# Kernel optimization log

Measured on AMD Instinct MI355X. Metric: run time of the kernel, lower is better.

## Reference

```python
import jax, jax.numpy as jnp
import numpy as np

B, S, H = 2, 1024, 2048
NH, NKV, HD = 16, 8, 128
N_REP = NH // NKV
EPS = 1e-6
ROPE_THETA = 1000000.0


def act_quant(x):
    # per-token int8 absmax quantization (BitNet)
    scale = 127.0 / jnp.clip(jnp.max(jnp.abs(x), axis=-1, keepdims=True), 1e-5, None)
    return jnp.clip(jnp.round(x * scale), -128.0, 127.0) / scale


def weight_quant(w):
    # ternary weight quantization via mean absmax (BitNet 1.58b)
    scale = 1.0 / jnp.clip(jnp.mean(jnp.abs(w)), 1e-5, None)
    return jnp.clip(jnp.round(w * scale), -1.0, 1.0) / scale


def bitlinear(x, w):
    # straight-through estimator: forward quantized, backward identity
    xq = x + jax.lax.stop_gradient(act_quant(x) - x)
    wq = w + jax.lax.stop_gradient(weight_quant(w) - w)
    return xq @ wq.T


def rmsnorm(x, weight):
    return weight * (x * jax.lax.rsqrt(jnp.mean(x * x, axis=-1, keepdims=True) + EPS))


def rotate_half(x):
    h = x.shape[-1] // 2
    return jnp.concatenate([-x[..., h:], x[..., :h]], axis=-1)


def setup_inputs() -> dict:
    key = jax.random.key(0)
    ks = jax.random.split(key, 6)
    x = jax.random.normal(ks[0], (B, S, H), jnp.float32)
    wq = jax.random.normal(ks[1], (NH * HD, H), jnp.float32) * 0.02
    wk = jax.random.normal(ks[2], (NKV * HD, H), jnp.float32) * 0.02
    wv = jax.random.normal(ks[3], (NKV * HD, H), jnp.float32) * 0.02
    wo = jax.random.normal(ks[4], (H, NH * HD), jnp.float32) * 0.02
    qn = jnp.ones((HD,), jnp.float32)
    kn = jnp.ones((HD,), jnp.float32)
    # real RoPE tables: [S, HD]
    inv_freq = 1.0 / (ROPE_THETA ** (jnp.arange(0, HD, 2, dtype=jnp.float32) / HD))
    freqs = jnp.outer(jnp.arange(S, dtype=jnp.float32), inv_freq)
    emb = jnp.concatenate([freqs, freqs], axis=-1)
    return dict(x=x, cos=jnp.cos(emb), sin=jnp.sin(emb),
                wq=wq, wk=wk, wv=wv, wo=wo, qn=qn, kn=kn)


def reference(x, cos, sin, wq, wk, wv, wo, qn, kn):
    b, s, _ = x.shape
    q = bitlinear(x, wq).reshape(b, s, NH, HD)
    k = bitlinear(x, wk).reshape(b, s, NKV, HD)
    v = bitlinear(x, wv).reshape(b, s, NKV, HD)
    # per-head QK RMSNorm
    q = rmsnorm(q, qn)
    k = rmsnorm(k, kn)
    # RoPE: cos/sin [S, HD] -> unsqueeze head dim -> [S, 1, HD]
    c = cos[:, None, :]
    sn = sin[:, None, :]
    q = q * c + rotate_half(q) * sn
    k = k * c + rotate_half(k) * sn
    # GQA expand: [b,s,NKV,HD] -> [b,s,NH,HD], adjacent copies per kv head
    k = jnp.repeat(k, N_REP, axis=2)
    v = jnp.repeat(v, N_REP, axis=2)
    # to [b, h, s, d]
    q = q.transpose(0, 2, 1, 3)
    k = k.transpose(0, 2, 1, 3)
    v = v.transpose(0, 2, 1, 3)
    scores = jnp.einsum('bhqd,bhkd->bhqk', q, k) / np.float32(np.sqrt(HD))
    causal = jnp.tril(jnp.ones((s, s), bool))
    scores = jnp.where(causal, scores, jnp.finfo(scores.dtype).min)
    probs = jax.nn.softmax(scores, axis=-1)
    out = jnp.einsum('bhqk,bhkd->bhqd', probs, v)
    out = out.transpose(0, 2, 1, 3).reshape(b, s, NH * HD)
    return bitlinear(out, wo)
```

## Files before the change

### kernel.cpp

```cpp
#include <hip/hip_runtime.h>
#include <hip/hip_bf16.h>

#define TT   2048
#define HH   2048
#define SEQ  1024
#define NHQ  16
#define NKVH 8
#define HDD  128

typedef __attribute__((ext_vector_type(8))) short short8;
typedef __attribute__((ext_vector_type(4))) float f32x4;
typedef __attribute__((ext_vector_type(4))) int int4v;
typedef _Float16 half8 __attribute__((ext_vector_type(8)));

static __device__ __forceinline__ unsigned short f2h(float f) {
  union { _Float16 h; unsigned short u; } c;
  c.h = (_Float16)f;
  return c.u;
}
static __device__ __forceinline__ half8 s2h(short8 v) {
  union { short8 s; half8 h; } c;
  c.s = v;
  return c.h;
}

#define GLD_LDS16(gp, lp)                                                        \
  __builtin_amdgcn_global_load_lds(                                              \
      (const __attribute__((address_space(1))) void*)(const void*)(gp),          \
      (__attribute__((address_space(3))) void*)(void*)(lp), 16, 0, 0)

__global__ __launch_bounds__(256) void k_quant_stats(const float* __restrict__ x,
                                                     signed char* __restrict__ xq,
                                                     float* __restrict__ as_inv,
                                                     const float* __restrict__ wq,
                                                     const float* __restrict__ wk,
                                                     const float* __restrict__ wv,
                                                     const float* __restrict__ wo,
                                                     double* __restrict__ part) {
  int tid = threadIdx.x;
  int wave = tid >> 6, lane = tid & 63;
  __shared__ double redd[256];
  __shared__ float wred[4];

  if (blockIdx.x < 2048) {
    int row = blockIdx.x;
    const float4* xr4 = (const float4*)(x + (size_t)row * HH);
    float4 a = xr4[tid * 2], b = xr4[tid * 2 + 1];
    float am = fmaxf(fmaxf(fmaxf(fabsf(a.x), fabsf(a.y)), fmaxf(fabsf(a.z), fabsf(a.w))),
                     fmaxf(fmaxf(fabsf(b.x), fabsf(b.y)), fmaxf(fabsf(b.z), fabsf(b.w))));
#pragma unroll
    for (int o = 32; o; o >>= 1) am = fmaxf(am, __shfl_xor(am, o));
    if (lane == 0) wred[wave] = am;
    __syncthreads();
    am = fmaxf(fmaxf(wred[0], wred[1]), fmaxf(wred[2], wred[3]));
    am = fmaxf(am, 1e-5f);
    if (tid == 0) as_inv[row] = am / 127.f;
    float scale = 127.f / am;
    float vals[8] = {a.x, a.y, a.z, a.w, b.x, b.y, b.z, b.w};
    unsigned int u0 = 0, u1 = 0;
#pragma unroll
    for (int j = 0; j < 4; ++j) {
      int q = (int)fminf(fmaxf(rintf(vals[j] * scale), -128.f), 127.f);
      u0 |= (unsigned int)(q & 255) << (8 * j);
    }
#pragma unroll
    for (int j = 0; j < 4; ++j) {
      int q = (int)fminf(fmaxf(rintf(vals[4 + j] * scale), -128.f), 127.f);
      u1 |= (unsigned int)(q & 255) << (8 * j);
    }
    uint2 uu; uu.x = u0; uu.y = u1;
    ((uint2*)(xq + (size_t)row * HH))[tid] = uu;
  } else {
    int idx = blockIdx.x - 2048;
    int wid = idx >> 8, sub = idx & 255;
    const float* w = (wid == 0) ? wq : (wid == 1) ? wk : (wid == 2) ? wv : wo;
    int nq = ((wid == 0 || wid == 3) ? 4194304 : 2097152) >> 2;
    double s = 0.0;
    for (int i = sub * 256 + tid; i < nq; i += 256 * 256) {
      float4 v = ((const float4*)w)[i];
      s += (double)fabsf(v.x) + (double)fabsf(v.y) + (double)fabsf(v.z) + (double)fabsf(v.w);
    }
    redd[tid] = s;
    __syncthreads();
    for (int st = 128; st > 0; st >>= 1) {
      if (tid < st) redd[tid] += redd[tid + st];
      __syncthreads();
    }
    if (tid == 0) part[wid * 256 + sub] = redd[0];
  }
}

__global__ __launch_bounds__(256) void k_wquant_all(const float* __restrict__ wq,
                                                    const float* __restrict__ wk,
                                                    const float* __restrict__ wv,
                                                    signed char* __restrict__ wqk,
                                                    signed char* __restrict__ wvt,
                                                    const double* __restrict__ part,
                                                    float* __restrict__ wsc) {
  int tid = threadIdx.x;
  int wave = tid >> 6, lane = tid & 63;
  __shared__ double wred[4][4];
  __shared__ float s_wsc[4];
  const double nvals[4] = {4194304.0, 2097152.0, 2097152.0, 4194304.0};
#pragma unroll
  for (int w = 0; w < 4; ++w) {
    double s = part[w * 256 + tid];
#pragma unroll
    for (int o = 32; o; o >>= 1) s += __shfl_xor(s, o);
    if (lane == 0) wred[w][wave] = s;
  }
  __syncthreads();
  if (tid < 4) {
    double s = (wred[tid][0] + wred[tid][1]) + (wred[tid][2] + wred[tid][3]);
    float v = fmaxf((float)(s / nvals[tid]), 1e-5f);
    s_wsc[tid] = v;
    if (blockIdx.x == 0) wsc[tid] = v;
  }
  __syncthreads();
  float inv0 = 1.f / s_wsc[0], inv1 = 1.f / s_wsc[1], inv2 = 1.f / s_wsc[2];

  const int NQ = 2097152;
  for (int qi = blockIdx.x * 256 + tid; qi < NQ; qi += gridDim.x * 256) {
    const float* src; signed char* dst; float inv; int off;
    if (qi < 1048576)      { src = wq; dst = wqk;           off = qi;           inv = inv0; }
    else if (qi < 1572864) { src = wk; dst = wqk + 4194304; off = qi - 1048576; inv = inv1; }
    else                   { src = wv; dst = wvt;           off = qi - 1572864; inv = inv2; }
    float4 v = ((const float4*)src)[off];
    unsigned int u = 0;
    float vv[4] = {v.x, v.y, v.z, v.w};
#pragma unroll
    for (int j = 0; j < 4; ++j) {
      int q = (int)fminf(fmaxf(rintf(vv[j] * inv), -1.f), 1.f);
      u |= (unsigned int)(q & 255) << (8 * j);
    }
    ((unsigned int*)dst)[off] = u;
  }
}

__global__ __launch_bounds__(256) void k_gemm_i8(const signed char* __restrict__ A0,
                                                 const signed char* __restrict__ B0,
                                                 const signed char* __restrict__ B1,
                                                 unsigned short* __restrict__ dh,
                                                 const float* __restrict__ asx,
                                                 const float* __restrict__ wsc,
                                                 const float* __restrict__ qn,
                                                 const float* __restrict__ kn,
                                                 const float* __restrict__ cs,
                                                 const float* __restrict__ sn,
                                                 unsigned short* __restrict__ qf,
                                                 unsigned short* __restrict__ kf) {
  const int K = HH;
  __shared__ signed char As[2][16384];
  __shared__ signed char Bs[2][16384];
  int tid = threadIdx.x;
  int wave = tid >> 6, lane = tid & 63, l15 = lane & 15, g = lane >> 4;
  int wm = wave >> 1, wn = wave & 1;

  int gid = (blockIdx.x & 7) * 64 + (blockIdx.x >> 3);
  const signed char *Ap, *Bp;
  int bm, bn, mode;
  if (gid < 384) { mode = 0; bm = (gid / 24) * 128; bn = (gid % 24) * 128; Ap = A0; Bp = B0; }
  else { mode = 1; int vid = gid - 384; bm = (vid >> 4) * 128; bn = (vid & 15) * 128; Ap = B1; Bp = A0; }

#define GSTAGE(K0, BUF)                                                               \
  {                                                                                   \
    _Pragma("unroll")                                                                 \
    for (int r = 0; r < 4; ++r) {                                                     \
      int c = r * 256 + tid;                                                          \
      int row = c >> 3;                                                               \
      int kk2 = ((c & 7) << 4) ^ ((row & 7) << 4);                                    \
      GLD_LDS16(Ap + (size_t)(bm + row) * K + (K0) + kk2, As[BUF] + c * 16);          \
      GLD_LDS16(Bp + (size_t)(bn + row) * K + (K0) + kk2, Bs[BUF] + c * 16);          \
    }                                                                                 \
  }

  int4v acc[4][4] = {};
  GSTAGE(0, 0);
  asm volatile("s_waitcnt vmcnt(0)" ::: "memory");
  __builtin_amdgcn_s_barrier();
  __builtin_amdgcn_sched_barrier(0);

  int buf = 0;
  for (int k0 = 0; k0 < K; k0 += 128) {
    bool more = (k0 + 128 < K);
    if (more) GSTAGE(k0 + 128, buf ^ 1);
#pragma unroll
    for (int ks = 0; ks < 2; ++ks) {
      int4v af[4], bf[4];
#pragma unroll
      for (int i = 0; i < 4; ++i) {
        int ra = wm * 64 + i * 16 + l15;
        af[i] = *(const int4v*)&As[buf][ra * 128 + ((ks * 64 + g * 16) ^ ((ra & 7) << 4))];
        int rb = (mode == 0) ? (wn * 32 + (i & 1) * 16 + (i >> 1) * 64 + l15)
                             : (wn * 64 + i * 16 + l15);
        bf[i] = *(const int4v*)&Bs[buf][rb * 128 + ((ks * 64 + g * 16) ^ ((rb & 7) << 4))];
      }
      __builtin_amdgcn_s_setprio(1);
#pragma unroll
      for (int mi = 0; mi < 4; ++mi)
#pragma unroll
        for (int ni = 0; ni < 4; ++ni)
          acc[mi][ni] = __builtin_amdgcn_mfma_i32_16x16x64_i8(af[mi], bf[ni], acc[mi][ni], 0, 0, 0);
      __builtin_amdgcn_s_setprio(0);
    }
    asm volatile("s_waitcnt vmcnt(0)" ::: "memory");
    __builtin_amdgcn_s_barrier();
    __builtin_amdgcn_sched_barrier(0);
    buf ^= 1;
  }
#undef GSTAGE

  if (mode == 0) {
    bool isq = (bn < 2048);
    int hh = isq ? (bn >> 7) : ((bn - 2048) >> 7);
    float wN = isq ? wsc[0] : wsc[1];
    float ps = isq ? 0.12751743075f : 1.0f;
    const float* nw = isq ? qn : kn;
    unsigned short* oh = isq ? qf : kf;
    int nhp = isq ? NHQ : NKVH;
    float* S = (float*)&As[0][0];
    __syncthreads();
#pragma unroll
    for (int mi = 0; mi < 4; ++mi) {
#pragma unroll
      for (int rr = 0; rr < 4; ++rr) {
        int tok = bm + wm * 64 + mi * 16 + 4 * g + rr;
        float rs = asx[tok] * wN;
        float ssum = 0.f;
#pragma unroll
        for (int ni = 0; ni < 4; ++ni) {
          float v = (float)acc[mi][ni][rr] * rs;
          ssum += v * v;
        }
        ssum += __shfl_xor(ssum, 1); ssum += __shfl_xor(ssum, 2);
        ssum += __shfl_xor(ssum, 4); ssum += __shfl_xor(ssum, 8);
        if (l15 == 0) S[wn * 128 + wm * 64 + mi * 16 + 4 * g + rr] = ssum;
      }
    }
    __syncthreads();
#pragma unroll
    for (int mi = 0; mi < 4; ++mi) {
#pragma unroll
      for (int rr = 0; rr < 4; ++rr) {
        int rloc = wm * 64 + mi * 16 + 4 * g + rr;
        int tok = bm + rloc;
        float rs = asx[tok] * wN;
        float inv = rsqrtf((S[rloc] + S[128 + rloc]) * (1.f / 128.f) + 1e-6f);
        int s = tok & (SEQ - 1);
        float nv[4];
#pragma unroll
        for (int ni = 0; ni < 4; ++ni) {
          int d = wn * 32 + (ni & 1) * 16 + (ni >> 1) * 64 + l15;
          nv[ni] = nw[d] * ((float)acc[mi][ni][rr] * rs) * inv;
        }
#pragma unroll
        for (int ni = 0; ni < 4; ++ni) {
          int d = wn * 32 + (ni & 1) * 16 + (ni >> 1) * 64 + l15;
          float oo = nv[ni ^ 2];
          float rh = (ni < 2) ? -oo : oo;
          float res = (nv[ni] * cs[s * 128 + d] + rh * sn[s * 128 + d]) * ps;
          size_t oi = ((size_t)tok * nhp + hh) * 128 + d;
          oh[oi] = f2h(res);
        }
      }
    }
  } else {
    float w2 = wsc[2];
#pragma unroll
    for (int mi = 0; mi < 4; ++mi) {
#pragma unroll
      for (int rr = 0; rr < 4; ++rr) {
        int crow = bm + wm * 64 + mi * 16 + 4 * g + rr;
#pragma unroll
        for (int ni = 0; ni < 4; ++ni) {
          int ccol = bn + wn * 64 + ni * 16 + l15;
          float v = (float)acc[mi][ni][rr] * asx[ccol] * w2;
          size_t ad = ((size_t)((ccol >> 10) * 1024 + crow)) * 1024 + (ccol & 1023);
          dh[ad] = f2h(v);
        }
      }
    }
  }
}

__global__ __launch_bounds__(256) void k_gemm_o(const signed char* __restrict__ A,
                                                const signed char* __restrict__ B,
                                                float* __restrict__ d0,
                                                const float* __restrict__ asx,
                                                const float* __restrict__ wsc) {
  const int K = HH;
  __shared__ signed char As[2][16384];
  __shared__ signed char Bs[2][8192];
  int tid = threadIdx.x;
  int wave = tid >> 6, lane = tid & 63, l15 = lane & 15, g = lane >> 4;
  int gid = (blockIdx.x & 7) * 64 + (blockIdx.x >> 3);
  int bm = (gid >> 5) * 128, bn = (gid & 31) * 64;

#define OSTAGE(K0, BUF)                                                               \
  {                                                                                   \
    _Pragma("unroll")                                                                 \
    for (int r = 0; r < 4; ++r) {                                                     \
      int c = r * 256 + tid;                                                          \
      int row = c >> 3;                                                               \
      int kk2 = ((c & 7) << 4) ^ ((row & 7) << 4);                                    \
      GLD_LDS16(A + (size_t)(bm + row) * K + (K0) + kk2, As[BUF] + c * 16);           \
    }                                                                                 \
    _Pragma("unroll")                                                                 \
    for (int r = 0; r < 2; ++r) {                                                     \
      int c = r * 256 + tid;                                                          \
      int row = c >> 3;                                                               \
      int kk2 = ((c & 7) << 4) ^ ((row & 7) << 4);                                    \
      GLD_LDS16(B + (size_t)(bn + row) * K + (K0) + kk2, Bs[BUF] + c * 16);           \
    }                                                                                 \
  }

  int4v acc[2][4] = {};
  OSTAGE(0, 0);
  asm volatile("s_waitcnt vmcnt(0)" ::: "memory");
  __builtin_amdgcn_s_barrier();
  __builtin_amdgcn_sched_barrier(0);

  int buf = 0;
  for (int k0 = 0; k0 < K; k0 += 128) {
    bool more = (k0 + 128 < K);
    if (more) OSTAGE(k0 + 128, buf ^ 1);
#pragma unroll
    for (int ks = 0; ks < 2; ++ks) {
      int4v af[2], bf[4];
#pragma unroll
      for (int i = 0; i < 2; ++i) {
        int ra = wave * 32 + i * 16 + l15;
        af[i] = *(const int4v*)&As[buf][ra * 128 + ((ks * 64 + g * 16) ^ ((ra & 7) << 4))];
      }
#pragma unroll
      for (int n = 0; n < 4; ++n) {
        int rb = n * 16 + l15;
        bf[n] = *(const int4v*)&Bs[buf][rb * 128 + ((ks * 64 + g * 16) ^ ((rb & 7) << 4))];
      }
      __builtin_amdgcn_s_setprio(1);
#pragma unroll
      for (int mi = 0; mi < 2; ++mi)
#pragma unroll
        for (int ni = 0; ni < 4; ++ni)
          acc[mi][ni] = __builtin_amdgcn_mfma_i32_16x16x64_i8(af[mi], bf[ni], acc[mi][ni], 0, 0, 0);
      __builtin_amdgcn_s_setprio(0);
    }
    asm volatile("s_waitcnt vmcnt(0)" ::: "memory");
    __builtin_amdgcn_s_barrier();
    __builtin_amdgcn_sched_barrier(0);
    buf ^= 1;
  }
#undef OSTAGE

  float w3 = wsc[3];
#pragma unroll
  for (int mi = 0; mi < 2; ++mi) {
#pragma unroll
    for (int rr = 0; rr < 4; ++rr) {
      int crow = bm + wave * 32 + mi * 16 + 4 * g + rr;
      float rs = asx[crow] * w3;
#pragma unroll
      for (int ni = 0; ni < 4; ++ni) {
        int ccol = bn + ni * 16 + l15;
        d0[(size_t)crow * 2048 + ccol] = (float)acc[mi][ni][rr] * rs;
      }
    }
  }
}

__global__ __launch_bounds__(256) void k_actquant(const float* __restrict__ x,
                                                  signed char* __restrict__ xq,
                                                  float* __restrict__ as_inv) {
  int row = blockIdx.x, tid = threadIdx.x;
  int wave = tid >> 6, lane = tid & 63;
  const float4* xr4 = (const float4*)(x + (size_t)row * HH);
  float4 a = xr4[tid * 2], b = xr4[tid * 2 + 1];
  float am = fmaxf(fmaxf(fmaxf(fabsf(a.x), fabsf(a.y)), fmaxf(fabsf(a.z), fabsf(a.w))),
                   fmaxf(fmaxf(fabsf(b.x), fabsf(b.y)), fmaxf(fabsf(b.z), fabsf(b.w))));
#pragma unroll
  for (int o = 32; o; o >>= 1) am = fmaxf(am, __shfl_xor(am, o));
  __shared__ float wred[4];
  if (lane == 0) wred[wave] = am;
  __syncthreads();
  am = fmaxf(fmaxf(wred[0], wred[1]), fmaxf(wred[2], wred[3]));
  am = fmaxf(am, 1e-5f);
  if (tid == 0) as_inv[row] = am / 127.f;
  float scale = 127.f / am;
  float vals[8] = {a.x, a.y, a.z, a.w, b.x, b.y, b.z, b.w};
  unsigned int u0 = 0, u1 = 0;
#pragma unroll
  for (int j = 0; j < 4; ++j) {
    int q = (int)fminf(fmaxf(rintf(vals[j] * scale), -128.f), 127.f);
    u0 |= (unsigned int)(q & 255) << (8 * j);
  }
#pragma unroll
  for (int j = 0; j < 4; ++j) {
    int q = (int)fminf(fmaxf(rintf(vals[4 + j] * scale), -128.f), 127.f);
    u1 |= (unsigned int)(q & 255) << (8 * j);
  }
  uint2 uu; uu.x = u0; uu.y = u1;
  ((uint2*)(xq + (size_t)row * HH))[tid] = uu;
}

__global__ __launch_bounds__(256) void k_attn_mfma(const unsigned short* __restrict__ qfp,
                                                   const unsigned short* __restrict__ kfp,
                                                   const unsigned short* __restrict__ vfp,
                                                   float* __restrict__ o,
                                                   const float* __restrict__ wsc,
                                                   const float* __restrict__ wo_f32,
                                                   signed char* __restrict__ wot) {
  int tid = threadIdx.x;
  if (blockIdx.x >= 512) {
    int bx = blockIdx.x - 512;
    float inv = 1.f / wsc[3];
    for (int qi = bx * 256 + tid; qi < 1048576; qi += 128 * 256) {
      float4 v = ((const float4*)wo_f32)[qi];
      unsigned int u = 0;
      float vv[4] = {v.x, v.y, v.z, v.w};
#pragma unroll
      for (int j = 0; j < 4; ++j) {
        int q = (int)fminf(fmaxf(rintf(vv[j] * inv), -1.f), 1.f);
        u |= (unsigned int)(q & 255) << (8 * j);
      }
      ((unsigned int*)wot)[qi] = u;
    }
    return;
  }

  int chunk = blockIdx.x & 7, j = blockIdx.x >> 3;
  int qt, yyi;
  if (j < 32) { qt = 15 - (j >> 2); yyi = j & 3; }
  else        { qt = (j - 32) >> 2; yyi = (j - 32) & 3; }
  int yy = (chunk << 2) + yyi;
  int b = yy >> 4, h = yy & 15, kvh = h >> 1;
  int wave = tid >> 6, lane = tid & 63;
  int l15 = lane & 15, g = lane >> 4;
  int q0w = qt * 64 + wave * 16;
  int qglob = q0w + l15;

  __shared__ unsigned short Kf[3][4096];
  __shared__ unsigned short Vf[3][4096];
  __shared__ unsigned short Plds[4][16][36];

  half8 qf[4];
  {
    const unsigned short* qb = qfp + ((size_t)(b * SEQ + qglob) * NHQ + h) * HDD + g * 8;
#pragma unroll
    for (int c = 0; c < 4; ++c) qf[c] = s2h(*(const short8*)(qb + c * 32));
  }
  half8 vones;
#pragma unroll
  for (int c = 0; c < 8; ++c) vones[c] = (_Float16)1.0f;

#define STAGE(KV0N, BUF)                                                              \
  {                                                                                   \
    int c0 = wave * 64 + lane;                                                        \
    _Pragma("unroll")                                                                 \
    for (int tch = 0; tch < 2; ++tch) {                                               \
      int c = tch * 256 + c0;                                                         \
      int ki = c >> 4, jb = (c & 15) << 4;                                            \
      int js = jb ^ ((ki & 7) << 4);                                                  \
      size_t kbase = ((size_t)(b * SEQ + (KV0N) + ki) * NKVH + kvh) * HDD;            \
      GLD_LDS16((const char*)(kfp + kbase) + js, &Kf[BUF][c * 8]);                    \
      int d = c >> 2, jv = (c & 3) << 4;                                              \
      int jvs = jv ^ ((d & 3) << 4);                                                  \
      size_t vbase = ((size_t)(b * 1024 + kvh * 128 + d)) * SEQ + (KV0N);             \
      GLD_LDS16((const char*)(vfp + vbase) + jvs, &Vf[BUF][c * 8]);                   \
    }                                                                                 \
  }

  f32x4 acc[9] = {};
  float m_run = -INFINITY;
  int nkv = 2 * qt + 2;

  STAGE(0, 0);
  STAGE(32, 1);
  asm volatile("s_waitcnt vmcnt(4) lgkmcnt(0)" ::: "memory");
  __builtin_amdgcn_s_barrier();
  __builtin_amdgcn_sched_barrier(0);

  int cur = 0, nxt = 1, nx2 = 2;
  for (int kv = 0; kv < nkv; ++kv) {
    int kv0 = kv * 32;
    bool more = (kv + 2 < nkv);
    if (more) STAGE(kv0 + 64, nx2);
    bool active = (kv0 <= q0w + 15);
    if (active) {
      const char* Kb = (const char*)&Kf[cur][0];
      const char* Vb = (const char*)&Vf[cur][0];
      float sc[2][4];
      __builtin_amdgcn_s_setprio(1);
#pragma unroll
      for (int t = 0; t < 2; ++t) {
        int row = 16 * t + l15;
        int rbyte = row * 256, sw = (row & 7) << 4;
        f32x4 s = {0.f, 0.f, 0.f, 0.f};
#pragma unroll
        for (int c = 0; c < 4; ++c) {
          int off = rbyte + ((c * 64 + g * 16) ^ sw);
          half8 kf8 = s2h(*(const short8*)(Kb + off));
          s = __builtin_amdgcn_mfma_f32_16x16x32_f16(kf8, qf[c], s, 0, 0, 0);
        }
#pragma unroll
        for (int r = 0; r < 4; ++r) sc[t][r] = s[r];
      }
      __builtin_amdgcn_s_setprio(0);
      if (kv0 + 31 > q0w) {
#pragma unroll
        for (int t = 0; t < 2; ++t)
#pragma unroll
          for (int r = 0; r < 4; ++r)
            if (kv0 + 16 * t + 4 * g + r > qglob) sc[t][r] = -INFINITY;
      }
      float pmax = -INFINITY;
#pragma unroll
      for (int t = 0; t < 2; ++t)
#pragma unroll
        for (int r = 0; r < 4; ++r) pmax = fmaxf(pmax, sc[t][r]);
      if (!__all(pmax <= m_run + 10.f)) {
        pmax = fmaxf(pmax, __shfl_xor(pmax, 16));
        pmax = fmaxf(pmax, __shfl_xor(pmax, 32));
        float mnew = fmaxf(m_run, pmax);
        float corr = exp2f(m_run - mnew);
        m_run = mnew;
        float corro[4];
#pragma unroll
        for (int r = 0; r < 4; ++r) corro[r] = __shfl(corr, 4 * g + r);
#pragma unroll
        for (int dt = 0; dt < 9; ++dt)
#pragma unroll
          for (int r = 0; r < 4; ++r) acc[dt][r] *= corro[r];
      }
      unsigned short ph[2][4];
#pragma unroll
      for (int t = 0; t < 2; ++t)
#pragma unroll
        for (int r = 0; r < 4; ++r)
          ph[t][r] = f2h(exp2f(sc[t][r] - m_run));
      ushort4 wh;
#pragma unroll
      for (int t = 0; t < 2; ++t) {
        wh.x = ph[t][0]; wh.y = ph[t][1]; wh.z = ph[t][2]; wh.w = ph[t][3];
        *(ushort4*)&Plds[wave][l15][16 * t + 4 * g] = wh;
      }
      half8 pa = s2h(*(const short8*)&Plds[wave][l15][8 * g]);
      __builtin_amdgcn_s_setprio(1);
#pragma unroll
      for (int dt = 0; dt < 8; ++dt) {
        int d = dt * 16 + l15;
        int off = d * 64 + ((g * 16) ^ ((d & 3) << 4));
        half8 vf8 = s2h(*(const short8*)(Vb + off));
        acc[dt] = __builtin_amdgcn_mfma_f32_16x16x32_f16(pa, vf8, acc[dt], 0, 0, 0);
      }
      acc[8] = __builtin_amdgcn_mfma_f32_16x16x32_f16(pa, vones, acc[8], 0, 0, 0);
      __builtin_amdgcn_s_setprio(0);
    }
    if (more) { asm volatile("s_waitcnt vmcnt(4)" ::: "memory"); }
    else      { asm volatile("s_waitcnt vmcnt(0)" ::: "memory"); }
    __builtin_amdgcn_s_barrier();
    __builtin_amdgcn_sched_barrier(0);
    int t0 = cur; cur = nxt; nxt = nx2; nx2 = t0;
  }
#undef STAGE

  float linv[4];
#pragma unroll
  for (int r = 0; r < 4; ++r) linv[r] = 1.f / acc[8][r];
#pragma unroll
  for (int r = 0; r < 4; ++r) {
    size_t orow = ((size_t)(b * SEQ + q0w + 4 * g + r) * NHQ + h) * HDD + l15;
#pragma unroll
    for (int dt = 0; dt < 8; ++dt)
      o[orow + dt * 16] = acc[dt][r] * linv[r];
  }
}

extern "C" void kernel_launch(void* const* d_in, const int* in_sizes, int n_in,
                              void* d_out, int out_size, void* d_ws, size_t ws_size,
                              hipStream_t stream) {
  const float* x  = (const float*)d_in[0];
  const float* cs = (const float*)d_in[1];
  const float* sn = (const float*)d_in[2];
  const float* wq = (const float*)d_in[3];
  const float* wk = (const float*)d_in[4];
  const float* wv = (const float*)d_in[5];
  const float* wo = (const float*)d_in[6];
  const float* qn = (const float*)d_in[7];
  const float* kn = (const float*)d_in[8];
  float* out = (float*)d_out;
  char* ws = (char*)d_ws;

  const size_t MB = 1024 * 1024;
  size_t o_xq  = 0;
  size_t o_wqk = 4  * MB;
  size_t o_wvt = 10 * MB;
  size_t o_wot = 12 * MB;
  size_t o_vt  = 16 * MB;
  size_t o_qf  = 20 * MB;
  size_t o_kf  = 28 * MB;
  size_t o_ao  = 32 * MB;
  size_t o_aq  = 48 * MB;
  size_t o_as  = 52 * MB;
  size_t o_as2 = o_as  + 8192;
  size_t o_prt = o_as2 + 8192;
  size_t o_wsc = o_prt + 8192;

  signed char* xq  = (signed char*)(ws + o_xq);
  signed char* wqk = (signed char*)(ws + o_wqk);
  signed char* wvt = (signed char*)(ws + o_wvt);
  signed char* wot = (signed char*)(ws + o_wot);
  unsigned short* vt = (unsigned short*)(ws + o_vt);
  unsigned short* qf = (unsigned short*)(ws + o_qf);
  unsigned short* kf = (unsigned short*)(ws + o_kf);
  float* ao = (float*)(ws + o_ao);
  signed char* aq = (signed char*)(ws + o_aq);
  float* asx = (float*)(ws + o_as);
  float* as2 = (float*)(ws + o_as2);
  double* prt = (double*)(ws + o_prt);
  float* wsc = (float*)(ws + o_wsc);

  k_quant_stats<<<3072, 256, 0, stream>>>(x, xq, asx, wq, wk, wv, wo, prt);

  k_wquant_all<<<1024, 256, 0, stream>>>(wq, wk, wv, wqk, wvt, prt, wsc);

  k_gemm_i8<<<512, 256, 0, stream>>>(xq, wqk, wvt, vt, asx, wsc,
                                     qn, kn, cs, sn, qf, kf);

  k_attn_mfma<<<640, 256, 0, stream>>>(qf, kf, vt, ao, wsc, wo, wot);

  k_actquant<<<TT, 256, 0, stream>>>(ao, aq, as2);
  k_gemm_o<<<512, 256, 0, stream>>>(aq, wot, out, as2, wsc);
}
```

Before: 118.1 us.

## Widen attention KV tile to 64 keys with double buffering

The flash-attention loop now processes 64 keys per iteration instead of 32. It double-buffers K/V tiles in LDS in place of triple-buffering 32-key tiles, and the V layout and swizzle are adjusted to 128-byte rows. This halves the number of loop iterations, barriers and softmax rescale checks, and each P fragment now feeds two MFMAs per output tile. In exchange the loop waits for the whole next-tile load (vmcnt(0)) every iteration, which overlaps compute and loads less, and the extra LDS and register use may lower occupancy. A no-op edit to the GEMM epilogue index is also included.

```diff
diff --git a/kernel.cpp b/kernel.cpp
--- a/kernel.cpp
+++ b/kernel.cpp
@@ -362,7 +362,7 @@
 #pragma unroll
       for (int ni = 0; ni < 4; ++ni) {
         int ccol = bn + ni * 16 + l15;
-        d0[(size_t)crow * 2048 + ccol] = (float)acc[mi][ni][rr] * rs;
+        d0[(size_t)crow * 2048 + ccol] = (float)acc[ni == 0 ? mi : mi][ni][rr] * rs;
       }
     }
   }
@@ -438,9 +438,9 @@
   int q0w = qt * 64 + wave * 16;
   int qglob = q0w + l15;
 
-  __shared__ unsigned short Kf[3][4096];
-  __shared__ unsigned short Vf[3][4096];
-  __shared__ unsigned short Plds[4][16][36];
+  __shared__ unsigned short Kf[2][8192];
+  __shared__ unsigned short Vf[2][8192];
+  __shared__ unsigned short Plds[4][16][72];
 
   half8 qf[4];
   {
@@ -452,18 +452,17 @@
 #pragma unroll
   for (int c = 0; c < 8; ++c) vones[c] = (_Float16)1.0f;
 
-#define STAGE(KV0N, BUF)                                                              \
+#define STAGE64(KV0N, BUF)                                                            \
   {                                                                                   \
-    int c0 = wave * 64 + lane;                                                        \
     _Pragma("unroll")                                                                 \
-    for (int tch = 0; tch < 2; ++tch) {                                               \
-      int c = tch * 256 + c0;                                                         \
+    for (int tch = 0; tch < 4; ++tch) {                                               \
+      int c = tch * 256 + tid;                                                        \
       int ki = c >> 4, jb = (c & 15) << 4;                                            \
       int js = jb ^ ((ki & 7) << 4);                                                  \
       size_t kbase = ((size_t)(b * SEQ + (KV0N) + ki) * NKVH + kvh) * HDD;            \
       GLD_LDS16((const char*)(kfp + kbase) + js, &Kf[BUF][c * 8]);                    \
-      int d = c >> 2, jv = (c & 3) << 4;                                              \
-      int jvs = jv ^ ((d & 3) << 4);                                                  \
+      int d = c >> 3, jv = (c & 7) << 4;                                              \
+      int jvs = jv ^ ((d & 7) << 4);                                                  \
       size_t vbase = ((size_t)(b * 1024 + kvh * 128 + d)) * SEQ + (KV0N);             \
       GLD_LDS16((const char*)(vfp + vbase) + jvs, &Vf[BUF][c * 8]);                   \
     }                                                                                 \
@@ -471,27 +470,26 @@
 
   f32x4 acc[9] = {};
   float m_run = -INFINITY;
-  int nkv = 2 * qt + 2;
-
-  STAGE(0, 0);
-  STAGE(32, 1);
-  asm volatile("s_waitcnt vmcnt(4) lgkmcnt(0)" ::: "memory");
+  int nkv = qt + 1;
+
+  STAGE64(0, 0);
+  asm volatile("s_waitcnt vmcnt(0) lgkmcnt(0)" ::: "memory");
   __builtin_amdgcn_s_barrier();
   __builtin_amdgcn_sched_barrier(0);
 
-  int cur = 0, nxt = 1, nx2 = 2;
+  int buf = 0;
   for (int kv = 0; kv < nkv; ++kv) {
-    int kv0 = kv * 32;
-    bool more = (kv + 2 < nkv);
-    if (more) STAGE(kv0 + 64, nx2);
+    int kv0 = kv * 64;
+    bool more = (kv + 1 < nkv);
+    if (more) STAGE64(kv0 + 64, buf ^ 1);
     bool active = (kv0 <= q0w + 15);
     if (active) {
-      const char* Kb = (const char*)&Kf[cur][0];
-      const char* Vb = (const char*)&Vf[cur][0];
-      float sc[2][4];
+      const char* Kb = (const char*)&Kf[buf][0];
+      const char* Vb = (const char*)&Vf[buf][0];
+      float sc[4][4];
       __builtin_amdgcn_s_setprio(1);
 #pragma unroll
-      for (int t = 0; t < 2; ++t) {
+      for (int t = 0; t < 4; ++t) {
         int row = 16 * t + l15;
         int rbyte = row * 256, sw = (row & 7) << 4;
         f32x4 s = {0.f, 0.f, 0.f, 0.f};
@@ -505,16 +503,16 @@
         for (int r = 0; r < 4; ++r) sc[t][r] = s[r];
       }
       __builtin_amdgcn_s_setprio(0);
-      if (kv0 + 31 > q0w) {
-#pragma unroll
-        for (int t = 0; t < 2; ++t)
+      if (kv0 + 63 > q0w) {
+#pragma unroll
+        for (int t = 0; t < 4; ++t)
 #pragma unroll
           for (int r = 0; r < 4; ++r)
             if (kv0 + 16 * t + 4 * g + r > qglob) sc[t][r] = -INFINITY;
       }
       float pmax = -INFINITY;
 #pragma unroll
-      for (int t = 0; t < 2; ++t)
+      for (int t = 0; t < 4; ++t)
 #pragma unroll
         for (int r = 0; r < 4; ++r) pmax = fmaxf(pmax, sc[t][r]);
       if (!__all(pmax <= m_run + 10.f)) {
@@ -531,37 +529,37 @@
 #pragma unroll
           for (int r = 0; r < 4; ++r) acc[dt][r] *= corro[r];
       }
-      unsigned short ph[2][4];
-#pragma unroll
-      for (int t = 0; t < 2; ++t)
-#pragma unroll
-        for (int r = 0; r < 4; ++r)
-          ph[t][r] = f2h(exp2f(sc[t][r] - m_run));
       ushort4 wh;
 #pragma unroll
-      for (int t = 0; t < 2; ++t) {
-        wh.x = ph[t][0]; wh.y = ph[t][1]; wh.z = ph[t][2]; wh.w = ph[t][3];
+      for (int t = 0; t < 4; ++t) {
+        wh.x = f2h(exp2f(sc[t][0] - m_run));
+        wh.y = f2h(exp2f(sc[t][1] - m_run));
+        wh.z = f2h(exp2f(sc[t][2] - m_run));
+        wh.w = f2h(exp2f(sc[t][3] - m_run));
         *(ushort4*)&Plds[wave][l15][16 * t + 4 * g] = wh;
       }
-      half8 pa = s2h(*(const short8*)&Plds[wave][l15][8 * g]);
+      half8 pa0 = s2h(*(const short8*)&Plds[wave][l15][8 * g]);
+      half8 pa1 = s2h(*(const short8*)&Plds[wave][l15][32 + 8 * g]);
       __builtin_amdgcn_s_setprio(1);
 #pragma unroll
       for (int dt = 0; dt < 8; ++dt) {
         int d = dt * 16 + l15;
-        int off = d * 64 + ((g * 16) ^ ((d & 3) << 4));
-        half8 vf8 = s2h(*(const short8*)(Vb + off));
-        acc[dt] = __builtin_amdgcn_mfma_f32_16x16x32_f16(pa, vf8, acc[dt], 0, 0, 0);
-      }
-      acc[8] = __builtin_amdgcn_mfma_f32_16x16x32_f16(pa, vones, acc[8], 0, 0, 0);
+        int rbase = d * 128, sw = (d & 7) << 4;
+        half8 v0 = s2h(*(const short8*)(Vb + rbase + ((g * 16) ^ sw)));
+        half8 v1 = s2h(*(const short8*)(Vb + rbase + ((64 + g * 16) ^ sw)));
+        acc[dt] = __builtin_amdgcn_mfma_f32_16x16x32_f16(pa0, v0, acc[dt], 0, 0, 0);
+        acc[dt] = __builtin_amdgcn_mfma_f32_16x16x32_f16(pa1, v1, acc[dt], 0, 0, 0);
+      }
+      acc[8] = __builtin_amdgcn_mfma_f32_16x16x32_f16(pa0, vones, acc[8], 0, 0, 0);
+      acc[8] = __builtin_amdgcn_mfma_f32_16x16x32_f16(pa1, vones, acc[8], 0, 0, 0);
       __builtin_amdgcn_s_setprio(0);
     }
-    if (more) { asm volatile("s_waitcnt vmcnt(4)" ::: "memory"); }
-    else      { asm volatile("s_waitcnt vmcnt(0)" ::: "memory"); }
+    asm volatile("s_waitcnt vmcnt(0)" ::: "memory");
     __builtin_amdgcn_s_barrier();
     __builtin_amdgcn_sched_barrier(0);
-    int t0 = cur; cur = nxt; nxt = nx2; nx2 = t0;
-  }
-#undef STAGE
+    buf ^= 1;
+  }
+#undef STAGE64
 
   float linv[4];
 #pragma unroll
```

After: 108.6 us. -8.1%, faster.
